# Kernel tuning notes

Hardware: AMD Instinct MI355X
Metric: run time of the kernel (lower is better)

Reference implementation:

```python
import jax, jax.numpy as jnp
import numpy as np

EPS = 1e-5  # torch LayerNorm default eps

def _layernorm(x):
    mu = x.mean(axis=-1, keepdims=True)
    var = x.var(axis=-1, keepdims=True)  # biased, matches torch
    return (x - mu) / jnp.sqrt(var + EPS)

def setup_inputs() -> dict:
    key = jax.random.key(0)
    k1, k2, k3, k4, k5 = jax.random.split(key, 5)
    B, T, E, H = 8, 2048, 512, 8
    d = E // H
    return {
        "input1": jax.random.normal(k1, (B, T, E), dtype=jnp.float32),
        "Wq": jax.random.normal(k2, (H, d), dtype=jnp.float32) * 0.1,
        "Wk": jax.random.normal(k3, (H, d), dtype=jnp.float32) * 0.1,
        "Wv": jax.random.normal(k4, (H, d, d), dtype=jnp.float32) * 0.1,
        "Wm": jax.random.normal(k5, (E, E), dtype=jnp.float32) * 0.05,
    }

def reference(input1, Wq, Wk, Wv, Wm):
    B, T, E = input1.shape
    H, d = Wq.shape
    xn = _layernorm(input1)                       # norm1 over Embed_Dim
    xh = xn.reshape(B, T, H, d)                   # per-head slices of last dim
    # QLayer surrogates: scalar query/key per token, d-dim value per token
    Q = jnp.einsum('bthd,hd->bht', xh, Wq)        # [B,H,T]
    K = jnp.einsum('bthd,hd->bht', xh, Wk)        # [B,H,T]
    V = jnp.einsum('bthd,hde->bhte', xh, Wv)      # [B,H,T,d]
    # distance attention: A = -(Q_i - K_j)^2
    A = -(Q[:, :, :, None] - K[:, :, None, :]) ** 2   # [B,H,T,T]
    P = jax.nn.softmax(A / (d ** 0.5), axis=-1)
    O = jnp.einsum('bhts,bhse->bhte', P, V)       # [B,H,T,d]
    head_result = O.transpose(0, 2, 1, 3).reshape(B, T, E)  # concat heads
    return head_result @ Wm + input1              # merger + residual
```

## Files before the change

### kernel.cpp

```cpp
#include <hip/hip_runtime.h>

typedef __bf16 bf16x8 __attribute__((ext_vector_type(8)));
typedef short short8 __attribute__((ext_vector_type(8)));
typedef float f32x4 __attribute__((ext_vector_type(4)));

#define TT 2048
#define EE 512
#define NH 8
#define DD 64

#define QSCALE 0.36067376022224085f
#define CSCALE 0.18033688011112042f

__device__ __forceinline__ ushort f2bf(float f) {
  union { float f; unsigned u; } a; a.f = f;
  unsigned u = a.u;
  return (ushort)((u + 0x7FFFu + ((u >> 16) & 1u)) >> 16);
}

__global__ __launch_bounds__(256) void k_ln(
    const float* __restrict__ x, const float* __restrict__ Wq,
    const float* __restrict__ Wk,
    float* __restrict__ Q, float* __restrict__ K, ushort* __restrict__ xnb) {
  const int token = blockIdx.x * 4 + (threadIdx.x >> 6);
  const int l = threadIdx.x & 63;
  const float* xr = x + (size_t)token * EE + l * 8;
  float4 a = *(const float4*)xr;
  float4 c = *(const float4*)(xr + 4);
  float xv[8] = {a.x, a.y, a.z, a.w, c.x, c.y, c.z, c.w};
  float s = 0.f, s2 = 0.f;
#pragma unroll
  for (int i = 0; i < 8; i++) { s += xv[i]; s2 = fmaf(xv[i], xv[i], s2); }
#pragma unroll
  for (int o = 32; o; o >>= 1) { s += __shfl_xor(s, o); s2 += __shfl_xor(s2, o); }
  const float mean = s * (1.f / 512.f);
  const float var = s2 * (1.f / 512.f) - mean * mean;
  const float rstd = rsqrtf(var + 1e-5f);

  float xn[8];
  short8 ob;
#pragma unroll
  for (int i = 0; i < 8; i++) {
    xn[i] = (xv[i] - mean) * rstd;
    ob[i] = (short)f2bf(xn[i]);
  }
  *(short8*)(xnb + (size_t)token * EE + l * 8) = ob;

  const float* wq = Wq + l * 8;
  const float* wk = Wk + l * 8;
  float4 q1 = *(const float4*)wq, q2 = *(const float4*)(wq + 4);
  float4 k1 = *(const float4*)wk, k2 = *(const float4*)(wk + 4);
  float wqv[8] = {q1.x, q1.y, q1.z, q1.w, q2.x, q2.y, q2.z, q2.w};
  float wkv[8] = {k1.x, k1.y, k1.z, k1.w, k2.x, k2.y, k2.z, k2.w};
  float q = 0.f, k = 0.f;
#pragma unroll
  for (int i = 0; i < 8; i++) { q = fmaf(xn[i], wqv[i], q); k = fmaf(xn[i], wkv[i], k); }
#pragma unroll
  for (int o = 4; o; o >>= 1) { q += __shfl_xor(q, o); k += __shfl_xor(k, o); }
  if ((l & 7) == 0) {
    const int h = l >> 3;
    const int b = token >> 11, t = token & (TT - 1);
    const int bh = b * NH + h;
    Q[bh * TT + t] = q * QSCALE;
    K[bh * TT + t] = k;
  }
}

__global__ __launch_bounds__(256) void k_tr(const ushort* __restrict__ xnb,
                                            ushort* __restrict__ xnt) {
  const int bh = blockIdx.y;
  const int b = bh >> 3, h = bh & 7;
  const int t0 = blockIdx.x * 64;
  const int tid = threadIdx.x;
  __shared__ ushort tile[64][72];

  {
    const int i = tid >> 3, ec = (tid & 7) * 8;
    const ushort* src = xnb + (size_t)(b * TT + t0 + i) * EE + h * DD + ec;
    *(uint4*)&tile[i][ec] = *(const uint4*)src;
    *(uint4*)&tile[i + 32][ec] = *(const uint4*)(src + 32 * EE);
  }
  __syncthreads();
  {
    const int e = tid >> 3, chunk = tid & 7, tc = (tid & 7) * 8;
    union { uint4 v; ushort u[8]; } o0, o1;
#pragma unroll
    for (int i = 0; i < 8; i++) {
      o0.u[i] = tile[tc + i][e];
      o1.u[i] = tile[tc + i][e + 32];
    }
    const int soff = ((chunk ^ (e & 7)) << 3);
    ushort* dst = xnt + (size_t)(bh * DD + e) * TT + t0 + soff;
    *(uint4*)dst = o0.v;
    *(uint4*)(dst + (size_t)32 * TT) = o1.v;
  }
}

__global__ __launch_bounds__(256) void k_wvm(
    const float* __restrict__ Wv, const float* __restrict__ Wm,
    ushort* __restrict__ Wvmt) {
  const int k = blockIdx.x;
  const int h = k >> 6;
  const int tid = threadIdx.x;
  __shared__ float wv[64];
  if (tid < 64) wv[tid] = Wv[k * 64 + tid];
  __syncthreads();
  float a0 = 0.f, a1 = 0.f;
#pragma unroll 8
  for (int e = 0; e < 64; e++) {
    const float w = wv[e];
    const float* row = Wm + (size_t)(h * 64 + e) * EE;
    a0 = fmaf(w, row[tid], a0);
    a1 = fmaf(w, row[tid + 256], a1);
  }
  Wvmt[(size_t)tid * EE + k] = f2bf(a0);
  Wvmt[(size_t)(tid + 256) * EE + k] = f2bf(a1);
}

__global__ __launch_bounds__(256, 2) void k_attn(
    const float* __restrict__ Q, const float* __restrict__ K,
    const ushort* __restrict__ xnt, ushort* __restrict__ hr) {
  const int sw = (blockIdx.x & 7) * 64 + (blockIdx.x >> 3);
  const int bh = sw >> 3;
  const int q0 = (sw & 7) * 256;
  const int b = bh >> 3, h = bh & 7;
  const int tid = threadIdx.x;
  const int w = tid >> 6, l = tid & 63;
  const int l16 = l & 15, lhi = l >> 4;

  __shared__ float ks[TT];
  __shared__ float cs[TT];
  __shared__ ushort vt[2][64 * 64];

  {
    const float* Kb = K + bh * TT;
#pragma unroll
    for (int i = 0; i < 8; i++) {
      float kv = Kb[tid + i * 256];
      ks[tid + i * 256] = kv;
      cs[tid + i * 256] = -kv * kv * CSCALE;
    }
  }

  const ushort* Xs = xnt + (size_t)bh * (DD * TT);
  const int se = tid >> 3;
  const int sc = (tid & 7) * 8;
  uint4 st0, st1;

#define ISSUE_STAGE(jt_) do {                                                  \
    st0 = *(const uint4*)(Xs + (size_t)se * TT + (jt_) + sc);                  \
    st1 = *(const uint4*)(Xs + (size_t)(se + 32) * TT + (jt_) + sc);           \
  } while (0)

#define WRITE_STAGE(buf_) do {                                                 \
    *(uint4*)&vt[buf_][se * 64 + sc] = st0;                                    \
    *(uint4*)&vt[buf_][(se + 32) * 64 + sc] = st1;                             \
  } while (0)

  ISSUE_STAGE(0);
  WRITE_STAGE(0);
  __syncthreads();

  float qv[4];
#pragma unroll
  for (int f = 0; f < 4; f++) qv[f] = Q[bh * TT + q0 + w * 64 + f * 16 + l16];

  f32x4 acc[4][4];
  f32x4 accd[4];
#pragma unroll
  for (int f = 0; f < 4; f++) {
    accd[f] = (f32x4){0.f, 0.f, 0.f, 0.f};
#pragma unroll
    for (int c = 0; c < 4; c++) acc[f][c] = (f32x4){0.f, 0.f, 0.f, 0.f};
  }
  short8 onesbits = {0x3F80, 0x3F80, 0x3F80, 0x3F80, 0x3F80, 0x3F80, 0x3F80, 0x3F80};
  const bf16x8 ones = __builtin_bit_cast(bf16x8, onesbits);

  int p = 0;
  for (int jt = 0; jt < TT; jt += 64) {
    const bool more = (jt + 64) < TT;
    if (more) ISSUE_STAGE(jt + 64);

    __builtin_amdgcn_s_setprio(1);
#pragma unroll
    for (int kk = 0; kk < 2; kk++) {
      bf16x8 vf[4];
#pragma unroll
      for (int c = 0; c < 4; c++) {
        const int e = c * 16 + l16;
        vf[c] = *(const bf16x8*)&vt[p][e * 64 + (((kk * 4 + lhi) ^ (e & 7)) << 3)];
      }
      const int jb = jt + kk * 32 + lhi * 8;
      float4 ka = *(const float4*)&ks[jb];
      float4 kb2 = *(const float4*)&ks[jb + 4];
      float4 ca = *(const float4*)&cs[jb];
      float4 cb2 = *(const float4*)&cs[jb + 4];
      float kv8[8] = {ka.x, ka.y, ka.z, ka.w, kb2.x, kb2.y, kb2.z, kb2.w};
      float cv8[8] = {ca.x, ca.y, ca.z, ca.w, cb2.x, cb2.y, cb2.z, cb2.w};
#pragma unroll
      for (int f = 0; f < 4; f++) {
        bf16x8 pa;
#pragma unroll
        for (int i = 0; i < 8; i++)
          pa[i] = (__bf16)__builtin_amdgcn_exp2f(fmaf(qv[f], kv8[i], cv8[i]));
        accd[f] = __builtin_amdgcn_mfma_f32_16x16x32_bf16(pa, ones, accd[f], 0, 0, 0);
#pragma unroll
        for (int c = 0; c < 4; c++)
          acc[f][c] = __builtin_amdgcn_mfma_f32_16x16x32_bf16(pa, vf[c], acc[f][c], 0, 0, 0);
      }
    }
    __builtin_amdgcn_s_setprio(0);

    if (more) WRITE_STAGE(p ^ 1);
    __syncthreads();
    p ^= 1;
  }
#undef ISSUE_STAGE
#undef WRITE_STAGE

#pragma unroll
  for (int f = 0; f < 4; f++) {
#pragma unroll
    for (int r = 0; r < 4; r++) {
      const float rinv = 1.f / accd[f][r];
      const int qrow = q0 + w * 64 + f * 16 + lhi * 4 + r;
      const size_t base = ((size_t)(b * TT + qrow)) * EE + h * DD + l16;
#pragma unroll
      for (int c = 0; c < 4; c++)
        hr[base + c * 16] = f2bf(acc[f][c][r] * rinv);
    }
  }
}

__global__ __launch_bounds__(256, 2) void k_merge(
    const ushort* __restrict__ hr, const ushort* __restrict__ Wmt,
    const float* __restrict__ x, float* __restrict__ out) {
  const int n0 = blockIdx.x * 128;
  const int m0 = blockIdx.y * 128;
  const int tid = threadIdx.x;
  const int w = tid >> 6, l = tid & 63;
  const int l16 = l & 15, lhi = l >> 4;
  const int wm = w >> 1, wn = w & 1;

  __shared__ ushort As[2][128 * 72];
  __shared__ ushort Bs[2][128 * 72];
  f32x4 acc[4][4];
#pragma unroll
  for (int i = 0; i < 4; i++)
#pragma unroll
    for (int j = 0; j < 4; j++) acc[i][j] = (f32x4){0.f, 0.f, 0.f, 0.f};

  const int row = tid >> 1, half = tid & 1;
  const ushort* sa0 = hr + (size_t)(m0 + row) * EE + half * 32;
  const ushort* sb0 = Wmt + (size_t)(n0 + row) * EE + half * 32;

  {
    uint4* da = (uint4*)&As[0][row * 72 + half * 32];
    uint4* db = (uint4*)&Bs[0][row * 72 + half * 32];
#pragma unroll
    for (int i = 0; i < 4; i++) da[i] = *(const uint4*)(sa0 + i * 8);
#pragma unroll
    for (int i = 0; i < 4; i++) db[i] = *(const uint4*)(sb0 + i * 8);
  }
  __syncthreads();

  int p = 0;
  for (int k0 = 0; k0 < EE; k0 += 64) {
    const bool more = (k0 + 64) < EE;
    uint4 pa[4], pb[4];
    if (more) {
#pragma unroll
      for (int i = 0; i < 4; i++) pa[i] = *(const uint4*)(sa0 + k0 + 64 + i * 8);
#pragma unroll
      for (int i = 0; i < 4; i++) pb[i] = *(const uint4*)(sb0 + k0 + 64 + i * 8);
    }
#pragma unroll
    for (int kk = 0; kk < 2; kk++) {
      bf16x8 af[4], bfr[4];
#pragma unroll
      for (int mi = 0; mi < 4; mi++)
        af[mi] = *(const bf16x8*)&As[p][(wm * 64 + mi * 16 + l16) * 72 + kk * 32 + lhi * 8];
#pragma unroll
      for (int ni = 0; ni < 4; ni++)
        bfr[ni] = *(const bf16x8*)&Bs[p][(wn * 64 + ni * 16 + l16) * 72 + kk * 32 + lhi * 8];
#pragma unroll
      for (int mi = 0; mi < 4; mi++)
#pragma unroll
        for (int ni = 0; ni < 4; ni++)
          acc[mi][ni] = __builtin_amdgcn_mfma_f32_16x16x32_bf16(af[mi], bfr[ni], acc[mi][ni], 0, 0, 0);
    }
    if (more) {
      uint4* da = (uint4*)&As[p ^ 1][row * 72 + half * 32];
      uint4* db = (uint4*)&Bs[p ^ 1][row * 72 + half * 32];
#pragma unroll
      for (int i = 0; i < 4; i++) da[i] = pa[i];
#pragma unroll
      for (int i = 0; i < 4; i++) db[i] = pb[i];
    }
    __syncthreads();
    p ^= 1;
  }

#pragma unroll
  for (int mi = 0; mi < 4; mi++) {
#pragma unroll
    for (int r = 0; r < 4; r++) {
      const int grow = m0 + wm * 64 + mi * 16 + lhi * 4 + r;
#pragma unroll
      for (int ni = 0; ni < 4; ni++) {
        const int gcol = n0 + wn * 64 + ni * 16 + l16;
        size_t idx = (size_t)grow * EE + gcol;
        out[idx] = acc[mi][ni][r] + x[idx];
      }
    }
  }
}

extern "C" void kernel_launch(void* const* d_in, const int* in_sizes, int n_in,
                              void* d_out, int out_size, void* d_ws, size_t ws_size,
                              hipStream_t stream) {
  const float* x  = (const float*)d_in[0];
  const float* Wq = (const float*)d_in[1];
  const float* Wk = (const float*)d_in[2];
  const float* Wv = (const float*)d_in[3];
  const float* Wm = (const float*)d_in[4];
  float* out = (float*)d_out;

  char* ws = (char*)d_ws;
  float*  Qp   = (float*)(ws);
  float*  Kp   = (float*)(ws + 524288);
  ushort* xnb  = (ushort*)(ws + 1048576);
  ushort* hrp  = (ushort*)(ws + 1048576);
  ushort* xnt  = (ushort*)(ws + 17825792);
  ushort* Wvmt = (ushort*)(ws + 34603008);

  k_ln<<<4096, 256, 0, stream>>>(x, Wq, Wk, Qp, Kp, xnb);
  k_tr<<<dim3(TT / 64, 8 * NH), 256, 0, stream>>>(xnb, xnt);
  k_wvm<<<EE, 256, 0, stream>>>(Wv, Wm, Wvmt);
  k_attn<<<512, 256, 0, stream>>>(Qp, Kp, xnt, hrp);
  k_merge<<<dim3(EE / 128, (8 * TT) / 128), 256, 0, stream>>>(hrp, Wvmt, x, out);
}
```

Measured before the change: 123.9 us.

## Split attention key range in two blocks and combine partials in new kernel

Attention now splits the key/value sequence into two halves, launching 1024 blocks instead of 512. Each block writes unnormalized bf16 partial outputs and row-sum partials, and a new combine kernel adds the halves and normalizes. The aim is more parallelism and occupancy (launch bounds raised to 4 blocks/SM) on a 512-block grid that underfills the GPU. The cost is an extra kernel, extra bf16 rounding of the partials, and about 32MB more memory traffic. The merge GEMM also gets an XCD-aware block remap for better L2 locality.

Result: slower. 169.4 us (+36.7%).

```diff
diff --git a/kernel.cpp b/kernel.cpp
--- a/kernel.cpp
+++ b/kernel.cpp
@@ -16,6 +16,10 @@
   union { float f; unsigned u; } a; a.f = f;
   unsigned u = a.u;
   return (ushort)((u + 0x7FFFu + ((u >> 16) & 1u)) >> 16);
+}
+__device__ __forceinline__ float bf2f(ushort b) {
+  union { unsigned u; float f; } a; a.u = ((unsigned)b) << 16;
+  return a.f;
 }
 
 __global__ __launch_bounds__(256) void k_ln(
@@ -117,32 +121,36 @@
   Wvmt[(size_t)(tid + 256) * EE + k] = f2bf(a1);
 }
 
-__global__ __launch_bounds__(256, 2) void k_attn(
+__global__ __launch_bounds__(256, 4) void k_attn(
     const float* __restrict__ Q, const float* __restrict__ K,
-    const ushort* __restrict__ xnt, ushort* __restrict__ hr) {
-  const int sw = (blockIdx.x & 7) * 64 + (blockIdx.x >> 3);
-  const int bh = sw >> 3;
-  const int q0 = (sw & 7) * 256;
+    const ushort* __restrict__ xnt, ushort* __restrict__ op1,
+    ushort* __restrict__ op2, float* __restrict__ ps) {
+  const int sw = (blockIdx.x & 7) * 128 + (blockIdx.x >> 3);
+  const int bh = sw >> 4;
+  const int rem = sw & 15;
+  const int q0 = (rem >> 1) * 256;
+  const int jh = rem & 1;
+  const int jbase = jh * 1024;
   const int b = bh >> 3, h = bh & 7;
   const int tid = threadIdx.x;
   const int w = tid >> 6, l = tid & 63;
   const int l16 = l & 15, lhi = l >> 4;
 
-  __shared__ float ks[TT];
-  __shared__ float cs[TT];
+  __shared__ float ks[1024];
+  __shared__ float cs[1024];
   __shared__ ushort vt[2][64 * 64];
 
   {
-    const float* Kb = K + bh * TT;
-#pragma unroll
-    for (int i = 0; i < 8; i++) {
+    const float* Kb = K + bh * TT + jbase;
+#pragma unroll
+    for (int i = 0; i < 4; i++) {
       float kv = Kb[tid + i * 256];
       ks[tid + i * 256] = kv;
       cs[tid + i * 256] = -kv * kv * CSCALE;
     }
   }
 
-  const ushort* Xs = xnt + (size_t)bh * (DD * TT);
+  const ushort* Xs = xnt + (size_t)bh * (DD * TT) + jbase;
   const int se = tid >> 3;
   const int sc = (tid & 7) * 8;
   uint4 st0, st1;
@@ -177,8 +185,8 @@
   const bf16x8 ones = __builtin_bit_cast(bf16x8, onesbits);
 
   int p = 0;
-  for (int jt = 0; jt < TT; jt += 64) {
-    const bool more = (jt + 64) < TT;
+  for (int jt = 0; jt < 1024; jt += 64) {
+    const bool more = (jt + 64) < 1024;
     if (more) ISSUE_STAGE(jt + 64);
 
     __builtin_amdgcn_s_setprio(1);
@@ -218,25 +226,46 @@
 #undef ISSUE_STAGE
 #undef WRITE_STAGE
 
+  ushort* op = jh ? op2 : op1;
+  float* psh = ps + jh * (64 * TT);
 #pragma unroll
   for (int f = 0; f < 4; f++) {
 #pragma unroll
     for (int r = 0; r < 4; r++) {
-      const float rinv = 1.f / accd[f][r];
       const int qrow = q0 + w * 64 + f * 16 + lhi * 4 + r;
       const size_t base = ((size_t)(b * TT + qrow)) * EE + h * DD + l16;
 #pragma unroll
       for (int c = 0; c < 4; c++)
-        hr[base + c * 16] = f2bf(acc[f][c][r] * rinv);
-    }
-  }
+        op[base + c * 16] = f2bf(acc[f][c][r]);
+      if (l16 == 0) psh[bh * TT + qrow] = accd[f][r];
+    }
+  }
+}
+
+__global__ __launch_bounds__(256) void k_comb(
+    const ushort* op1, const ushort* op2, const float* __restrict__ ps,
+    ushort* hro) {
+  const size_t idx = ((size_t)blockIdx.x * 256 + threadIdx.x) * 8;
+  const int tok = (int)(idx >> 9), c = (int)(idx & 511);
+  const int b = tok >> 11, t = tok & (TT - 1), h = c >> 6;
+  const int q = (b * NH + h) * TT + t;
+  const float rinv = 1.f / (ps[q] + ps[64 * TT + q]);
+  short8 a = *(const short8*)(op1 + idx);
+  short8 bb = *(const short8*)(op2 + idx);
+  short8 o;
+#pragma unroll
+  for (int i = 0; i < 8; i++)
+    o[i] = (short)f2bf((bf2f((ushort)a[i]) + bf2f((ushort)bb[i])) * rinv);
+  *(short8*)(hro + idx) = o;
 }
 
 __global__ __launch_bounds__(256, 2) void k_merge(
     const ushort* __restrict__ hr, const ushort* __restrict__ Wmt,
     const float* __restrict__ x, float* __restrict__ out) {
-  const int n0 = blockIdx.x * 128;
-  const int m0 = blockIdx.y * 128;
+  const int fid = blockIdx.y * 4 + blockIdx.x;
+  const int xcd = fid & 7, idx = fid >> 3;
+  const int n0 = (idx & 3) * 128;
+  const int m0 = (xcd * 16 + (idx >> 2)) * 128;
   const int tid = threadIdx.x;
   const int w = tid >> 6, l = tid & 63;
   const int l16 = l & 15, lhi = l >> 4;
@@ -309,8 +338,8 @@
 #pragma unroll
       for (int ni = 0; ni < 4; ni++) {
         const int gcol = n0 + wn * 64 + ni * 16 + l16;
-        size_t idx = (size_t)grow * EE + gcol;
-        out[idx] = acc[mi][ni][r] + x[idx];
+        size_t idx2 = (size_t)grow * EE + gcol;
+        out[idx2] = acc[mi][ni][r] + x[idx2];
       }
     }
   }
@@ -330,13 +359,17 @@
   float*  Qp   = (float*)(ws);
   float*  Kp   = (float*)(ws + 524288);
   ushort* xnb  = (ushort*)(ws + 1048576);
+  ushort* op1  = (ushort*)(ws + 1048576);
   ushort* hrp  = (ushort*)(ws + 1048576);
   ushort* xnt  = (ushort*)(ws + 17825792);
-  ushort* Wvmt = (ushort*)(ws + 34603008);
+  ushort* op2  = (ushort*)(ws + 34603008);
+  float*  psp  = (float*)(ws + 51380224);
+  ushort* Wvmt = (ushort*)(ws + 52428800);
 
   k_ln<<<4096, 256, 0, stream>>>(x, Wq, Wk, Qp, Kp, xnb);
   k_tr<<<dim3(TT / 64, 8 * NH), 256, 0, stream>>>(xnb, xnt);
   k_wvm<<<EE, 256, 0, stream>>>(Wv, Wm, Wvmt);
-  k_attn<<<512, 256, 0, stream>>>(Qp, Kp, xnt, hrp);
+  k_attn<<<1024, 256, 0, stream>>>(Qp, Kp, xnt, op1, op2, psp);
+  k_comb<<<4096, 256, 0, stream>>>(op1, op2, psp, hrp);
   k_merge<<<dim3(EE / 128, (8 * TT) / 128), 256, 0, stream>>>(hrp, Wvmt, x, out);
 }
```

## Load V fragments directly from global in attention, halve query tile, remap merge blocks

Applied to the files above, without the earlier changes.

The attention kernel drops its LDS double-buffered staging of the transposed values and reads MFMA B-fragments straight from global memory (relying on L2/L1). The transpose kernel no longer XOR-swizzles its output to match that direct layout. Each block now handles 128 queries instead of 256 with 1024 blocks and a 4-blocks-per-CU bound, and the exp computation is split from the MFMA issue. The merge GEMM remaps block IDs so that tiles sharing rows land on the same XCD. In exchange, V is re-read from global by more blocks and global load latency is no longer hidden by explicit staging.

Result: slower. 189.9 us (+53.2%).

```diff
diff --git a/kernel.cpp b/kernel.cpp
--- a/kernel.cpp
+++ b/kernel.cpp
@@ -82,15 +82,14 @@
   }
   __syncthreads();
   {
-    const int e = tid >> 3, chunk = tid & 7, tc = (tid & 7) * 8;
+    const int e = tid >> 3, tc = (tid & 7) * 8;
     union { uint4 v; ushort u[8]; } o0, o1;
 #pragma unroll
     for (int i = 0; i < 8; i++) {
       o0.u[i] = tile[tc + i][e];
       o1.u[i] = tile[tc + i][e + 32];
     }
-    const int soff = ((chunk ^ (e & 7)) << 3);
-    ushort* dst = xnt + (size_t)(bh * DD + e) * TT + t0 + soff;
+    ushort* dst = xnt + (size_t)(bh * DD + e) * TT + t0 + tc;
     *(uint4*)dst = o0.v;
     *(uint4*)(dst + (size_t)32 * TT) = o1.v;
   }
@@ -117,12 +116,12 @@
   Wvmt[(size_t)(tid + 256) * EE + k] = f2bf(a1);
 }
 
-__global__ __launch_bounds__(256, 2) void k_attn(
+__global__ __launch_bounds__(256, 4) void k_attn(
     const float* __restrict__ Q, const float* __restrict__ K,
     const ushort* __restrict__ xnt, ushort* __restrict__ hr) {
-  const int sw = (blockIdx.x & 7) * 64 + (blockIdx.x >> 3);
-  const int bh = sw >> 3;
-  const int q0 = (sw & 7) * 256;
+  const int sw = (blockIdx.x & 7) * 128 + (blockIdx.x >> 3);
+  const int bh = sw >> 4;
+  const int q0 = (sw & 15) * 128;
   const int b = bh >> 3, h = bh & 7;
   const int tid = threadIdx.x;
   const int w = tid >> 6, l = tid & 63;
@@ -130,7 +129,6 @@
 
   __shared__ float ks[TT];
   __shared__ float cs[TT];
-  __shared__ ushort vt[2][64 * 64];
 
   {
     const float* Kb = K + bh * TT;
@@ -141,34 +139,16 @@
       cs[tid + i * 256] = -kv * kv * CSCALE;
     }
   }
-
-  const ushort* Xs = xnt + (size_t)bh * (DD * TT);
-  const int se = tid >> 3;
-  const int sc = (tid & 7) * 8;
-  uint4 st0, st1;
-
-#define ISSUE_STAGE(jt_) do {                                                  \
-    st0 = *(const uint4*)(Xs + (size_t)se * TT + (jt_) + sc);                  \
-    st1 = *(const uint4*)(Xs + (size_t)(se + 32) * TT + (jt_) + sc);           \
-  } while (0)
-
-#define WRITE_STAGE(buf_) do {                                                 \
-    *(uint4*)&vt[buf_][se * 64 + sc] = st0;                                    \
-    *(uint4*)&vt[buf_][(se + 32) * 64 + sc] = st1;                             \
-  } while (0)
-
-  ISSUE_STAGE(0);
-  WRITE_STAGE(0);
   __syncthreads();
 
-  float qv[4];
-#pragma unroll
-  for (int f = 0; f < 4; f++) qv[f] = Q[bh * TT + q0 + w * 64 + f * 16 + l16];
-
-  f32x4 acc[4][4];
-  f32x4 accd[4];
-#pragma unroll
-  for (int f = 0; f < 4; f++) {
+  float qv[2];
+  qv[0] = Q[bh * TT + q0 + w * 32 + l16];
+  qv[1] = Q[bh * TT + q0 + w * 32 + 16 + l16];
+
+  f32x4 acc[2][4];
+  f32x4 accd[2];
+#pragma unroll
+  for (int f = 0; f < 2; f++) {
     accd[f] = (f32x4){0.f, 0.f, 0.f, 0.f};
 #pragma unroll
     for (int c = 0; c < 4; c++) acc[f][c] = (f32x4){0.f, 0.f, 0.f, 0.f};
@@ -176,21 +156,22 @@
   short8 onesbits = {0x3F80, 0x3F80, 0x3F80, 0x3F80, 0x3F80, 0x3F80, 0x3F80, 0x3F80};
   const bf16x8 ones = __builtin_bit_cast(bf16x8, onesbits);
 
-  int p = 0;
+  const ushort* Xt = xnt + (size_t)bh * (DD * TT) + (size_t)l16 * TT;
+  const int jo = lhi * 8;
+
   for (int jt = 0; jt < TT; jt += 64) {
-    const bool more = (jt + 64) < TT;
-    if (more) ISSUE_STAGE(jt + 64);
-
-    __builtin_amdgcn_s_setprio(1);
+    bf16x8 vf0[4], vf1[4];
+#pragma unroll
+    for (int c = 0; c < 4; c++) {
+      const ushort* base = Xt + (size_t)c * 16 * TT + jt + jo;
+      vf0[c] = *(const bf16x8*)(base);
+      vf1[c] = *(const bf16x8*)(base + 32);
+    }
+
+    bf16x8 pa[2][2];
 #pragma unroll
     for (int kk = 0; kk < 2; kk++) {
-      bf16x8 vf[4];
-#pragma unroll
-      for (int c = 0; c < 4; c++) {
-        const int e = c * 16 + l16;
-        vf[c] = *(const bf16x8*)&vt[p][e * 64 + (((kk * 4 + lhi) ^ (e & 7)) << 3)];
-      }
-      const int jb = jt + kk * 32 + lhi * 8;
+      const int jb = jt + kk * 32 + jo;
       float4 ka = *(const float4*)&ks[jb];
       float4 kb2 = *(const float4*)&ks[jb + 4];
       float4 ca = *(const float4*)&cs[jb];
@@ -198,32 +179,34 @@
       float kv8[8] = {ka.x, ka.y, ka.z, ka.w, kb2.x, kb2.y, kb2.z, kb2.w};
       float cv8[8] = {ca.x, ca.y, ca.z, ca.w, cb2.x, cb2.y, cb2.z, cb2.w};
 #pragma unroll
-      for (int f = 0; f < 4; f++) {
-        bf16x8 pa;
+      for (int f = 0; f < 2; f++) {
 #pragma unroll
         for (int i = 0; i < 8; i++)
-          pa[i] = (__bf16)__builtin_amdgcn_exp2f(fmaf(qv[f], kv8[i], cv8[i]));
-        accd[f] = __builtin_amdgcn_mfma_f32_16x16x32_bf16(pa, ones, accd[f], 0, 0, 0);
+          pa[kk][f][i] = (__bf16)__builtin_amdgcn_exp2f(fmaf(qv[f], kv8[i], cv8[i]));
+      }
+    }
+
+    __builtin_amdgcn_s_setprio(1);
+#pragma unroll
+    for (int kk = 0; kk < 2; kk++) {
+#pragma unroll
+      for (int f = 0; f < 2; f++) {
+        accd[f] = __builtin_amdgcn_mfma_f32_16x16x32_bf16(pa[kk][f], ones, accd[f], 0, 0, 0);
 #pragma unroll
         for (int c = 0; c < 4; c++)
-          acc[f][c] = __builtin_amdgcn_mfma_f32_16x16x32_bf16(pa, vf[c], acc[f][c], 0, 0, 0);
+          acc[f][c] = __builtin_amdgcn_mfma_f32_16x16x32_bf16(
+              pa[kk][f], kk ? vf1[c] : vf0[c], acc[f][c], 0, 0, 0);
       }
     }
     __builtin_amdgcn_s_setprio(0);
-
-    if (more) WRITE_STAGE(p ^ 1);
-    __syncthreads();
-    p ^= 1;
-  }
-#undef ISSUE_STAGE
-#undef WRITE_STAGE
-
-#pragma unroll
-  for (int f = 0; f < 4; f++) {
+  }
+
+#pragma unroll
+  for (int f = 0; f < 2; f++) {
 #pragma unroll
     for (int r = 0; r < 4; r++) {
       const float rinv = 1.f / accd[f][r];
-      const int qrow = q0 + w * 64 + f * 16 + lhi * 4 + r;
+      const int qrow = q0 + w * 32 + f * 16 + lhi * 4 + r;
       const size_t base = ((size_t)(b * TT + qrow)) * EE + h * DD + l16;
 #pragma unroll
       for (int c = 0; c < 4; c++)
@@ -235,8 +218,10 @@
 __global__ __launch_bounds__(256, 2) void k_merge(
     const ushort* __restrict__ hr, const ushort* __restrict__ Wmt,
     const float* __restrict__ x, float* __restrict__ out) {
-  const int n0 = blockIdx.x * 128;
-  const int m0 = blockIdx.y * 128;
+  const int fid = blockIdx.y * 4 + blockIdx.x;
+  const int xcd = fid & 7, idx = fid >> 3;
+  const int n0 = (idx & 3) * 128;
+  const int m0 = (xcd * 16 + (idx >> 2)) * 128;
   const int tid = threadIdx.x;
   const int w = tid >> 6, l = tid & 63;
   const int l16 = l & 15, lhi = l >> 4;
@@ -309,8 +294,8 @@
 #pragma unroll
       for (int ni = 0; ni < 4; ni++) {
         const int gcol = n0 + wn * 64 + ni * 16 + l16;
-        size_t idx = (size_t)grow * EE + gcol;
-        out[idx] = acc[mi][ni][r] + x[idx];
+        size_t idx2 = (size_t)grow * EE + gcol;
+        out[idx2] = acc[mi][ni][r] + x[idx2];
       }
     }
   }
@@ -337,6 +322,6 @@
   k_ln<<<4096, 256, 0, stream>>>(x, Wq, Wk, Qp, Kp, xnb);
   k_tr<<<dim3(TT / 64, 8 * NH), 256, 0, stream>>>(xnb, xnt);
   k_wvm<<<EE, 256, 0, stream>>>(Wv, Wm, Wvmt);
-  k_attn<<<512, 256, 0, stream>>>(Qp, Kp, xnt, hrp);
+  k_attn<<<1024, 256, 0, stream>>>(Qp, Kp, xnt, hrp);
   k_merge<<<dim3(EE / 128, (8 * TT) / 128), 256, 0, stream>>>(hrp, Wvmt, x, out);
 }
```

## Fuse layernorm with per-head transpose and remap merge tiles across XCDs

Applied to the files above, without the earlier changes.

Merges the layernorm kernel and the transpose kernel into one 1024-thread kernel. Each block normalizes 64 tokens into a shared-memory tile and then writes the per-head transposed bf16 layout straight to global memory, which removes the intermediate xnb buffer round trip and one launch. The merge GEMM block index is also remapped so that each XCD handles a contiguous set of row tiles, with the aim of better L2 locality. The cost is that the fused kernel launches only 256 large blocks with 66KB of shared memory each, which lowers parallelism, and its transposed reads from shared memory may hit bank conflicts.

After: 119.2 us. 1.04x faster.

```diff
diff --git a/kernel.cpp b/kernel.cpp
--- a/kernel.cpp
+++ b/kernel.cpp
@@ -18,81 +18,75 @@
   return (ushort)((u + 0x7FFFu + ((u >> 16) & 1u)) >> 16);
 }
 
-__global__ __launch_bounds__(256) void k_ln(
+__global__ __launch_bounds__(1024) void k_lnt(
     const float* __restrict__ x, const float* __restrict__ Wq,
     const float* __restrict__ Wk,
-    float* __restrict__ Q, float* __restrict__ K, ushort* __restrict__ xnb) {
-  const int token = blockIdx.x * 4 + (threadIdx.x >> 6);
-  const int l = threadIdx.x & 63;
-  const float* xr = x + (size_t)token * EE + l * 8;
-  float4 a = *(const float4*)xr;
-  float4 c = *(const float4*)(xr + 4);
-  float xv[8] = {a.x, a.y, a.z, a.w, c.x, c.y, c.z, c.w};
-  float s = 0.f, s2 = 0.f;
-#pragma unroll
-  for (int i = 0; i < 8; i++) { s += xv[i]; s2 = fmaf(xv[i], xv[i], s2); }
-#pragma unroll
-  for (int o = 32; o; o >>= 1) { s += __shfl_xor(s, o); s2 += __shfl_xor(s2, o); }
-  const float mean = s * (1.f / 512.f);
-  const float var = s2 * (1.f / 512.f) - mean * mean;
-  const float rstd = rsqrtf(var + 1e-5f);
-
-  float xn[8];
-  short8 ob;
-#pragma unroll
-  for (int i = 0; i < 8; i++) {
-    xn[i] = (xv[i] - mean) * rstd;
-    ob[i] = (short)f2bf(xn[i]);
-  }
-  *(short8*)(xnb + (size_t)token * EE + l * 8) = ob;
-
-  const float* wq = Wq + l * 8;
-  const float* wk = Wk + l * 8;
-  float4 q1 = *(const float4*)wq, q2 = *(const float4*)(wq + 4);
-  float4 k1 = *(const float4*)wk, k2 = *(const float4*)(wk + 4);
-  float wqv[8] = {q1.x, q1.y, q1.z, q1.w, q2.x, q2.y, q2.z, q2.w};
-  float wkv[8] = {k1.x, k1.y, k1.z, k1.w, k2.x, k2.y, k2.z, k2.w};
-  float q = 0.f, k = 0.f;
-#pragma unroll
-  for (int i = 0; i < 8; i++) { q = fmaf(xn[i], wqv[i], q); k = fmaf(xn[i], wkv[i], k); }
-#pragma unroll
-  for (int o = 4; o; o >>= 1) { q += __shfl_xor(q, o); k += __shfl_xor(k, o); }
-  if ((l & 7) == 0) {
-    const int h = l >> 3;
-    const int b = token >> 11, t = token & (TT - 1);
-    const int bh = b * NH + h;
-    Q[bh * TT + t] = q * QSCALE;
-    K[bh * TT + t] = k;
-  }
-}
-
-__global__ __launch_bounds__(256) void k_tr(const ushort* __restrict__ xnb,
-                                            ushort* __restrict__ xnt) {
-  const int bh = blockIdx.y;
-  const int b = bh >> 3, h = bh & 7;
+    float* __restrict__ Q, float* __restrict__ K, ushort* __restrict__ xnt) {
+  const int tid = threadIdx.x;
+  const int wv = tid >> 6, l = tid & 63;
   const int t0 = blockIdx.x * 64;
-  const int tid = threadIdx.x;
-  __shared__ ushort tile[64][72];
+  __shared__ ushort tile[64][520];
+
+#pragma unroll
+  for (int it = 0; it < 4; it++) {
+    const int tl = wv * 4 + it;
+    const int token = t0 + tl;
+    const float* xr = x + (size_t)token * EE + l * 8;
+    float4 a = *(const float4*)xr;
+    float4 c = *(const float4*)(xr + 4);
+    float xv[8] = {a.x, a.y, a.z, a.w, c.x, c.y, c.z, c.w};
+    float s = 0.f, s2 = 0.f;
+#pragma unroll
+    for (int i = 0; i < 8; i++) { s += xv[i]; s2 = fmaf(xv[i], xv[i], s2); }
+#pragma unroll
+    for (int o = 32; o; o >>= 1) { s += __shfl_xor(s, o); s2 += __shfl_xor(s2, o); }
+    const float mean = s * (1.f / 512.f);
+    const float var = s2 * (1.f / 512.f) - mean * mean;
+    const float rstd = rsqrtf(var + 1e-5f);
+
+    float xn[8];
+    short8 ob;
+#pragma unroll
+    for (int i = 0; i < 8; i++) {
+      xn[i] = (xv[i] - mean) * rstd;
+      ob[i] = (short)f2bf(xn[i]);
+    }
+    *(short8*)&tile[tl][l * 8] = ob;
+
+    const float* wq = Wq + l * 8;
+    const float* wk = Wk + l * 8;
+    float4 q1 = *(const float4*)wq, q2 = *(const float4*)(wq + 4);
+    float4 k1 = *(const float4*)wk, k2 = *(const float4*)(wk + 4);
+    float wqv[8] = {q1.x, q1.y, q1.z, q1.w, q2.x, q2.y, q2.z, q2.w};
+    float wkv[8] = {k1.x, k1.y, k1.z, k1.w, k2.x, k2.y, k2.z, k2.w};
+    float q = 0.f, k = 0.f;
+#pragma unroll
+    for (int i = 0; i < 8; i++) { q = fmaf(xn[i], wqv[i], q); k = fmaf(xn[i], wkv[i], k); }
+#pragma unroll
+    for (int o = 4; o; o >>= 1) { q += __shfl_xor(q, o); k += __shfl_xor(k, o); }
+    if ((l & 7) == 0) {
+      const int h = l >> 3;
+      const int b = token >> 11, t = token & (TT - 1);
+      const int bh = b * NH + h;
+      Q[bh * TT + t] = q * QSCALE;
+      K[bh * TT + t] = k;
+    }
+  }
+  __syncthreads();
 
   {
-    const int i = tid >> 3, ec = (tid & 7) * 8;
-    const ushort* src = xnb + (size_t)(b * TT + t0 + i) * EE + h * DD + ec;
-    *(uint4*)&tile[i][ec] = *(const uint4*)src;
-    *(uint4*)&tile[i + 32][ec] = *(const uint4*)(src + 32 * EE);
-  }
-  __syncthreads();
-  {
-    const int e = tid >> 3, chunk = tid & 7, tc = (tid & 7) * 8;
-    union { uint4 v; ushort u[8]; } o0, o1;
-#pragma unroll
-    for (int i = 0; i < 8; i++) {
-      o0.u[i] = tile[tc + i][e];
-      o1.u[i] = tile[tc + i][e + 32];
-    }
-    const int soff = ((chunk ^ (e & 7)) << 3);
-    ushort* dst = xnt + (size_t)(bh * DD + e) * TT + t0 + soff;
-    *(uint4*)dst = o0.v;
-    *(uint4*)(dst + (size_t)32 * TT) = o1.v;
+    const int h = tid >> 7, e = (tid >> 1) & 63, half = tid & 1;
+    const int b = t0 >> 11, trow = t0 & (TT - 1);
+    const int col = h * 64 + e;
+    ushort* rowp = xnt + (size_t)((b * NH + h) * DD + e) * TT + trow;
+#pragma unroll
+    for (int ch = 0; ch < 4; ch++) {
+      const int c_idx = half * 4 + ch;
+      union { uint4 v; ushort u[8]; } o;
+#pragma unroll
+      for (int i = 0; i < 8; i++) o.u[i] = tile[c_idx * 8 + i][col];
+      *(uint4*)(rowp + (((c_idx ^ (e & 7)) << 3))) = o.v;
+    }
   }
 }
 
@@ -235,8 +229,10 @@
 __global__ __launch_bounds__(256, 2) void k_merge(
     const ushort* __restrict__ hr, const ushort* __restrict__ Wmt,
     const float* __restrict__ x, float* __restrict__ out) {
-  const int n0 = blockIdx.x * 128;
-  const int m0 = blockIdx.y * 128;
+  const int fid = blockIdx.y * 4 + blockIdx.x;
+  const int xcd = fid & 7, idx = fid >> 3;
+  const int n0 = (idx & 3) * 128;
+  const int m0 = (xcd * 16 + (idx >> 2)) * 128;
   const int tid = threadIdx.x;
   const int w = tid >> 6, l = tid & 63;
   const int l16 = l & 15, lhi = l >> 4;
@@ -309,8 +305,8 @@
 #pragma unroll
       for (int ni = 0; ni < 4; ni++) {
         const int gcol = n0 + wn * 64 + ni * 16 + l16;
-        size_t idx = (size_t)grow * EE + gcol;
-        out[idx] = acc[mi][ni][r] + x[idx];
+        size_t idx2 = (size_t)grow * EE + gcol;
+        out[idx2] = acc[mi][ni][r] + x[idx2];
       }
     }
   }
@@ -329,13 +325,11 @@
   char* ws = (char*)d_ws;
   float*  Qp   = (float*)(ws);
   float*  Kp   = (float*)(ws + 524288);
-  ushort* xnb  = (ushort*)(ws + 1048576);
   ushort* hrp  = (ushort*)(ws + 1048576);
   ushort* xnt  = (ushort*)(ws + 17825792);
   ushort* Wvmt = (ushort*)(ws + 34603008);
 
-  k_ln<<<4096, 256, 0, stream>>>(x, Wq, Wk, Qp, Kp, xnb);
-  k_tr<<<dim3(TT / 64, 8 * NH), 256, 0, stream>>>(xnb, xnt);
+  k_lnt<<<256, 1024, 0, stream>>>(x, Wq, Wk, Qp, Kp, xnt);
   k_wvm<<<EE, 256, 0, stream>>>(Wv, Wm, Wvmt);
   k_attn<<<512, 256, 0, stream>>>(Qp, Kp, xnt, hrp);
   k_merge<<<dim3(EE / 128, (8 * TT) / 128), 256, 0, stream>>>(hrp, Wvmt, x, out);
```
